# Optimization experiments

Hardware: AMD Instinct MI355X
Metric: run time of the kernel (lower is better)

The kernel has to match this reference:

```python
import jax, jax.numpy as jnp
import numpy as np

B, C, H, W = 16, 3, 384, 1280
EPS = 1e-7


def setup_inputs() -> dict:
    key = jax.random.key(0)
    k1, k2, k3, k4 = jax.random.split(key, 4)
    source_image = jax.random.normal(k1, (B, C, H, W), jnp.float32)
    depth_map = jax.random.uniform(k2, (B, 1, H, W), jnp.float32, minval=0.1, maxval=80.0)
    pose = 0.05 * jax.random.normal(k3, (B, 6), jnp.float32)
    # realistic KITTI-style pinhole intrinsics, per-batch mild perturbation
    base = jnp.array([[0.58 * W, 0.0, 0.5 * W],
                      [0.0, 1.92 * H, 0.5 * H],
                      [0.0, 0.0, 1.0]], jnp.float32)
    noise = 1.0 + 0.01 * jax.random.normal(k4, (B, 3, 3), jnp.float32)
    intrinsic = base[None] * noise  # zero entries stay zero -> invertible
    return {"source_image": source_image, "depth_map": depth_map,
            "pose": pose, "intrinsic": intrinsic}


def rot_from_axisangle(aa):
    # aa: [B,3] -> [B,3,3] (Rodrigues)
    theta = jnp.linalg.norm(aa, axis=-1, keepdims=True)  # [B,1]
    axis = aa / (theta + EPS)
    c = jnp.cos(theta)
    s = jnp.sin(theta)
    t = 1.0 - c
    x, y, z = axis[:, 0:1], axis[:, 1:2], axis[:, 2:3]
    row0 = jnp.concatenate([t * x * x + c, t * x * y - s * z, t * z * x + s * y], axis=1)
    row1 = jnp.concatenate([t * x * y + s * z, t * y * y + c, t * y * z - s * x], axis=1)
    row2 = jnp.concatenate([t * z * x - s * y, t * y * z + s * x, t * z * z + c], axis=1)
    return jnp.stack([row0, row1, row2], axis=1)  # [B,3,3]


def bilinear_grid_sample(img, gx, gy):
    # img: [B,C,H,W]; gx,gy: [B,H,W] in [-1,1]; align_corners=True, padding zeros
    Bc, Cc, Hc, Wc = img.shape
    x = (gx + 1.0) * 0.5 * (Wc - 1)
    y = (gy + 1.0) * 0.5 * (Hc - 1)
    x0 = jnp.floor(x)
    y0 = jnp.floor(y)
    x1 = x0 + 1.0
    y1 = y0 + 1.0
    wx1 = x - x0
    wx0 = 1.0 - wx1
    wy1 = y - y0
    wy0 = 1.0 - wy1
    imgf = img.reshape(Bc, Cc, Hc * Wc)

    def gather(xi, yi):
        inb = ((xi >= 0) & (xi <= Wc - 1) & (yi >= 0) & (yi <= Hc - 1)).astype(img.dtype)
        xc = jnp.clip(xi, 0, Wc - 1).astype(jnp.int32)
        yc = jnp.clip(yi, 0, Hc - 1).astype(jnp.int32)
        idx = (yc * Wc + xc).reshape(Bc, 1, -1)
        vals = jnp.take_along_axis(imgf, jnp.broadcast_to(idx, (Bc, Cc, idx.shape[-1])), axis=2)
        return vals.reshape(Bc, Cc, Hc, Wc) * inb[:, None]

    out = (gather(x0, y0) * (wx0 * wy0)[:, None]
           + gather(x1, y0) * (wx1 * wy0)[:, None]
           + gather(x0, y1) * (wx0 * wy1)[:, None]
           + gather(x1, y1) * (wx1 * wy1)[:, None])
    return out


def reference(source_image, depth_map, pose, intrinsic):
    Bb, _, Hh, Ww = depth_map.shape
    # pixel grid, homogeneous [H,W,3] = (x, y, 1)
    ys, xs = jnp.meshgrid(jnp.arange(Hh, dtype=depth_map.dtype),
                          jnp.arange(Ww, dtype=depth_map.dtype), indexing='ij')
    pix = jnp.stack([xs, ys, jnp.ones_like(xs)], axis=-1)  # [H,W,3]
    # backproject: K^{-1} @ pix * depth
    inv_K = jnp.linalg.inv(intrinsic)  # [B,3,3]
    cam = jnp.einsum('bij,hwj->bhwi', inv_K, pix)  # [B,H,W,3]
    frustum = cam * jnp.transpose(depth_map, (0, 2, 3, 1))  # [B,H,W,3]
    # rigid transform
    R = rot_from_axisangle(pose[:, :3])  # [B,3,3]
    t = pose[:, 3:]  # [B,3]
    points = jnp.einsum('bij,bhwj->bhwi', R, frustum) + t[:, None, None, :]
    # project with K
    coord = jnp.einsum('bij,bhwj->bhwi', intrinsic, points)  # [B,H,W,3]
    z = coord[..., 2] + EPS
    px = coord[..., 0] / z
    py = coord[..., 1] / z
    gx = px / (Ww - 1) * 2.0 - 1.0
    gy = py / (Hh - 1) * 2.0 - 1.0
    return bilinear_grid_sample(source_image, gx, gy)
```

## Files before the change

kernel.cpp:

```cpp
#include <hip/hip_runtime.h>
#include <hip/hip_fp16.h>

#define B_ 16
#define C_ 3
#define H_ 384
#define W_ 1280
#define HW_ (H_*W_)
#define EPS_ 1e-7f

#define WP_ 1284
#define HP_ 386
#define NXCD_ 8

#define BANDS_ (W_/256)
#define RTILES_ (H_/2)
#define NBLK3_ (BANDS_*RTILES_*B_)
#define CPX3_  (NBLK3_/NXCD_)

#define PADPB_ (2*WP_ + 4*H_)
#define NPAD_  (B_*PADPB_)

typedef float v2f __attribute__((ext_vector_type(2)));
typedef float v4f __attribute__((ext_vector_type(4)));

__device__ __forceinline__ v2f load2(const float* p) {
  v2f r; __builtin_memcpy(&r, p, 8); return r;
}
__device__ __forceinline__ uint4 load16u(const void* p) {
  uint4 r; __builtin_memcpy(&r, p, 16); return r;
}
__device__ __forceinline__ v4f ntload4(const float* p) {
  return __builtin_nontemporal_load((const v4f*)p);
}
__device__ __forceinline__ void storent2(float* p, float a, float b) {
  v2f r; r.x = a; r.y = b;
  __builtin_nontemporal_store(r, (v2f*)p);
}
__device__ __forceinline__ unsigned pack2(float a, float b) {
  __half2 h = __floats2half2_rn(a, b);
  unsigned u; __builtin_memcpy(&u, &h, 4); return u;
}

__device__ __forceinline__ void mat3mul(const float* A, const float* Bm, float* C) {
  #pragma unroll
  for (int i = 0; i < 3; i++)
    #pragma unroll
    for (int j = 0; j < 3; j++)
      C[i*3+j] = A[i*3+0]*Bm[0*3+j] + A[i*3+1]*Bm[1*3+j] + A[i*3+2]*Bm[2*3+j];
}

__device__ void compute_MT(const float* __restrict__ pose,
                           const float* __restrict__ intr,
                           int b, float* M, float* T)
{
  float K[9];
  #pragma unroll
  for (int i = 0; i < 9; i++) K[i] = intr[b*9 + i];
  float aa0 = pose[b*6 + 0], aa1 = pose[b*6 + 1], aa2 = pose[b*6 + 2];
  float t0  = pose[b*6 + 3], t1  = pose[b*6 + 4], t2  = pose[b*6 + 5];

  float theta = sqrtf(aa0*aa0 + aa1*aa1 + aa2*aa2);
  float invn  = 1.0f / (theta + EPS_);
  float x = aa0*invn, y = aa1*invn, z = aa2*invn;
  float c = cosf(theta), s = sinf(theta), t = 1.0f - c;
  float R[9] = {
    t*x*x + c,   t*x*y - s*z, t*z*x + s*y,
    t*x*y + s*z, t*y*y + c,   t*y*z - s*x,
    t*z*x - s*y, t*y*z + s*x, t*z*z + c
  };

  float a = K[0], bb = K[1], cc = K[2];
  float d = K[3], e  = K[4], f  = K[5];
  float g = K[6], h  = K[7], ii = K[8];
  float A0 = e*ii - f*h, A1 = f*g - d*ii, A2 = d*h - e*g;
  float id = 1.0f / (a*A0 + bb*A1 + cc*A2);
  float iK[9] = {
    A0*id, (cc*h - bb*ii)*id, (bb*f - cc*e)*id,
    A1*id, (a*ii - cc*g)*id,  (cc*d - a*f)*id,
    A2*id, (bb*g - a*h)*id,   (a*e  - bb*d)*id
  };

  float KR[9];
  mat3mul(K, R, KR);
  mat3mul(KR, iK, M);
  T[0] = K[0]*t0 + K[1]*t1 + K[2]*t2;
  T[1] = K[3]*t0 + K[4]*t1 + K[5]*t2;
  T[2] = K[6]*t0 + K[7]*t1 + K[8]*t2;
}

__global__ __launch_bounds__(256) void pad_kernel(unsigned long long* __restrict__ ws)
{
  int tid = blockIdx.x * 256 + threadIdx.x;
  if (tid >= NPAD_) return;
  int b = tid / PADPB_;
  int k = tid - b * PADPB_;
  int row, col;
  if (k < WP_)            { row = 0;       col = k; }
  else if (k < 2*WP_)     { row = HP_ - 1; col = k - WP_; }
  else {
    int kk = k - 2*WP_;
    row = (kk >> 2) + 1;
    int c4 = kk & 3;
    col = (c4 < 2) ? c4 : (WP_ - 4 + c4);
  }
  ws[(size_t)(b * HP_ + row) * WP_ + col] = 0ULL;
}

__global__ __launch_bounds__(256) void repack_kernel(
    const float* __restrict__ src, uint4* __restrict__ ws)
{
  int tg = blockIdx.x * 256 + threadIdx.x;
  int b  = tg / (HW_/4);
  int rq = tg - b * (HW_/4);
  int p  = rq * 4;
  int y  = p / W_;
  int x  = p - y * W_;
  const float* s = src + (size_t)b * 3 * HW_ + p;
  v4f c0 = ntload4(s);
  v4f c1 = ntload4(s + HW_);
  v4f c2 = ntload4(s + 2*HW_);
  uint4 o0, o1;
  o0.x = pack2(c0.x, c1.x); o0.y = pack2(c2.x, 0.0f);
  o0.z = pack2(c0.y, c1.y); o0.w = pack2(c2.y, 0.0f);
  o1.x = pack2(c0.z, c1.z); o1.y = pack2(c2.z, 0.0f);
  o1.z = pack2(c0.w, c1.w); o1.w = pack2(c2.w, 0.0f);
  size_t slot = (size_t)(b * HP_ + y + 1) * WP_ + (x + 2);
  ws[slot >> 1]       = o0;
  ws[(slot >> 1) + 1] = o1;
}

__global__ __launch_bounds__(256) void warp2_kernel(
    const uint4* __restrict__ pk,
    const float* __restrict__ depth,
    const float* __restrict__ pose,
    const float* __restrict__ intr,
    float* __restrict__ out)
{
  __shared__ float sp[12];

  int l = blockIdx.x;
  int w = (l & (NXCD_-1)) * CPX3_ + (l >> 3);
  int rt   = w % RTILES_;
  int tmp  = w / RTILES_;
  int band = tmp % BANDS_;
  int b    = tmp / BANDS_;

  int t  = threadIdx.x;
  int rr = t >> 7;
  int cp = t & 127;
  int j0 = band * 256 + 2*cp;
  int i  = rt * 2 + rr;

  v2f dq = load2(depth + (size_t)b * HW_ + (size_t)i * W_ + j0);

  if (t == 0) {
    float M[9], T[3];
    compute_MT(pose, intr, b, M, T);
    #pragma unroll
    for (int k = 0; k < 9; k++) sp[k] = M[k];
    #pragma unroll
    for (int k = 0; k < 3; k++) sp[9 + k] = T[k];
  }
  __syncthreads();
  float m00 = sp[0], m01 = sp[1], m02 = sp[2];
  float m10 = sp[3], m11 = sp[4], m12 = sp[5];
  float m20 = sp[6], m21 = sp[7], m22 = sp[8];
  float T0  = sp[9], T1  = sp[10], T2 = sp[11];

  float yf = (float)i;
  float bx = m01*yf + m02;
  float by = m11*yf + m12;
  float bz = m21*yf + m22;

  const char* pkb = (const char*)pk;
  const float Wm1 = (float)(W_-1), Hm1 = (float)(H_-1);
  int rowbase = b * HP_;

  float xfA = (float)j0;
  float dA  = dq.x;
  float czA = (m20*xfA + bz)*dA + T2;
  float ivA = __builtin_amdgcn_rcpf(czA + EPS_);
  float pxA = ((m00*xfA + bx)*dA + T0) * ivA;
  float pyA = ((m10*xfA + by)*dA + T1) * ivA;
  float x0A = floorf(pxA), y0A = floorf(pyA);
  float fx1A = pxA - x0A, fx0A = 1.0f - fx1A;
  float fy1A = pyA - y0A, fy0A = 1.0f - fy1A;
  float wx0A = (x0A >= 0.0f      && x0A <= Wm1) ? fx0A : 0.0f;
  float wx1A = (x0A+1.0f >= 0.0f && x0A+1.0f <= Wm1) ? fx1A : 0.0f;
  float wy0A = (y0A >= 0.0f      && y0A <= Hm1) ? fy0A : 0.0f;
  float wy1A = (y0A+1.0f >= 0.0f && y0A+1.0f <= Hm1) ? fy1A : 0.0f;
  float w00A = wx0A*wy0A, w01A = wx1A*wy0A, w10A = wx0A*wy1A, w11A = wx1A*wy1A;
  int xbA = (int)fminf(fmaxf(x0A, -1.0f), Wm1);
  int ybA = (int)fminf(fmaxf(y0A, -1.0f), Hm1);
  size_t offA0 = ((size_t)(rowbase + ybA + 1) * WP_ + (xbA + 2)) * 8;

  float xfB = (float)(j0 + 1);
  float dB  = dq.y;
  float czB = (m20*xfB + bz)*dB + T2;
  float ivB = __builtin_amdgcn_rcpf(czB + EPS_);
  float pxB = ((m00*xfB + bx)*dB + T0) * ivB;
  float pyB = ((m10*xfB + by)*dB + T1) * ivB;
  float x0B = floorf(pxB), y0B = floorf(pyB);
  float fx1B = pxB - x0B, fx0B = 1.0f - fx1B;
  float fy1B = pyB - y0B, fy0B = 1.0f - fy1B;
  float wx0B = (x0B >= 0.0f      && x0B <= Wm1) ? fx0B : 0.0f;
  float wx1B = (x0B+1.0f >= 0.0f && x0B+1.0f <= Wm1) ? fx1B : 0.0f;
  float wy0B = (y0B >= 0.0f      && y0B <= Hm1) ? fy0B : 0.0f;
  float wy1B = (y0B+1.0f >= 0.0f && y0B+1.0f <= Hm1) ? fy1B : 0.0f;
  float w00B = wx0B*wy0B, w01B = wx1B*wy0B, w10B = wx0B*wy1B, w11B = wx1B*wy1B;
  int xbB = (int)fminf(fmaxf(x0B, -1.0f), Wm1);
  int ybB = (int)fminf(fmaxf(y0B, -1.0f), Hm1);
  size_t offB0 = ((size_t)(rowbase + ybB + 1) * WP_ + (xbB + 2)) * 8;

  uint4 RA0 = load16u(pkb + offA0);
  uint4 RA1 = load16u(pkb + offA0 + (size_t)WP_*8);
  uint4 RB0 = load16u(pkb + offB0);
  uint4 RB1 = load16u(pkb + offB0 + (size_t)WP_*8);
  __builtin_amdgcn_sched_barrier(0);

  float2 A00 = __half22float2(*(const __half2*)&RA0.x);
  float  A02 = __low2float  (*(const __half2*)&RA0.y);
  float2 A01 = __half22float2(*(const __half2*)&RA0.z);
  float  A03 = __low2float  (*(const __half2*)&RA0.w);
  float2 A10 = __half22float2(*(const __half2*)&RA1.x);
  float  A12 = __low2float  (*(const __half2*)&RA1.y);
  float2 A11 = __half22float2(*(const __half2*)&RA1.z);
  float  A13 = __low2float  (*(const __half2*)&RA1.w);
  float vA0 = A00.x*w00A + A01.x*w01A + A10.x*w10A + A11.x*w11A;
  float vA1 = A00.y*w00A + A01.y*w01A + A10.y*w10A + A11.y*w11A;
  float vA2 = A02  *w00A + A03  *w01A + A12  *w10A + A13  *w11A;

  float2 B00 = __half22float2(*(const __half2*)&RB0.x);
  float  B02 = __low2float  (*(const __half2*)&RB0.y);
  float2 B01 = __half22float2(*(const __half2*)&RB0.z);
  float  B03 = __low2float  (*(const __half2*)&RB0.w);
  float2 B10 = __half22float2(*(const __half2*)&RB1.x);
  float  B12 = __low2float  (*(const __half2*)&RB1.y);
  float2 B11 = __half22float2(*(const __half2*)&RB1.z);
  float  B13 = __low2float  (*(const __half2*)&RB1.w);
  float vB0 = B00.x*w00B + B01.x*w01B + B10.x*w10B + B11.x*w11B;
  float vB1 = B00.y*w00B + B01.y*w01B + B10.y*w10B + B11.y*w11B;
  float vB2 = B02  *w00B + B03  *w01B + B12  *w10B + B13  *w11B;

  size_t sb = (size_t)b * C_ * HW_;
  size_t op = (size_t)i * W_ + j0;
  storent2(out + sb + op,                   vA0, vB0);
  storent2(out + sb + HW_ + op,             vA1, vB1);
  storent2(out + sb + 2*(size_t)HW_ + op,   vA2, vB2);
}

__global__ __launch_bounds__(256) void warp_fb_kernel(
    const float* __restrict__ src,
    const float* __restrict__ depth,
    const float* __restrict__ pose,
    const float* __restrict__ intr,
    float* __restrict__ out)
{
  __shared__ float sp[12];
  int b = blockIdx.y;
  if (threadIdx.x == 0) {
    float M[9], T[3];
    compute_MT(pose, intr, b, M, T);
    #pragma unroll
    for (int k = 0; k < 9; k++) sp[k] = M[k];
    #pragma unroll
    for (int k = 0; k < 3; k++) sp[9 + k] = T[k];
  }
  __syncthreads();
  float m00 = sp[0], m01 = sp[1], m02 = sp[2];
  float m10 = sp[3], m11 = sp[4], m12 = sp[5];
  float m20 = sp[6], m21 = sp[7], m22 = sp[8];
  float T0  = sp[9], T1  = sp[10], T2 = sp[11];

  int p = blockIdx.x * 256 + threadIdx.x;
  int j = p % W_;
  int i = p / W_;

  float d  = depth[(size_t)b * HW_ + p];
  float xf = (float)j, yf = (float)i;
  float cx = (m00*xf + m01*yf + m02)*d + T0;
  float cy = (m10*xf + m11*yf + m12)*d + T1;
  float cz = (m20*xf + m21*yf + m22)*d + T2;
  float inv = 1.0f / (cz + EPS_);
  float px = cx * inv, py = cy * inv;

  float x0f = floorf(px), y0f = floorf(py);
  float x1f = x0f + 1.0f, y1f = y0f + 1.0f;
  float wx1 = px - x0f, wx0 = 1.0f - wx1;
  float wy1 = py - y0f, wy0 = 1.0f - wy1;
  float mx0 = (x0f >= 0.0f && x0f <= (float)(W_-1)) ? 1.0f : 0.0f;
  float mx1 = (x1f >= 0.0f && x1f <= (float)(W_-1)) ? 1.0f : 0.0f;
  float my0 = (y0f >= 0.0f && y0f <= (float)(H_-1)) ? 1.0f : 0.0f;
  float my1 = (y1f >= 0.0f && y1f <= (float)(H_-1)) ? 1.0f : 0.0f;
  int xc0 = (int)fminf(fmaxf(x0f, 0.0f), (float)(W_-1));
  int xc1 = (int)fminf(fmaxf(x1f, 0.0f), (float)(W_-1));
  int yc0 = (int)fminf(fmaxf(y0f, 0.0f), (float)(H_-1));
  int yc1 = (int)fminf(fmaxf(y1f, 0.0f), (float)(H_-1));
  float w00 = wx0*wy0*mx0*my0;
  float w01 = wx1*wy0*mx1*my0;
  float w10 = wx0*wy1*mx0*my1;
  float w11 = wx1*wy1*mx1*my1;
  int base = xc0 < (W_-2) ? xc0 : (W_-2);
  bool s0 = (xc0 == base);
  bool s1 = (xc1 == base + 1);
  float wax = (s0 ? w00 : 0.0f) + (s1 ? 0.0f : w01);
  float way = (s0 ? 0.0f : w00) + (s1 ? w01 : 0.0f);
  float wbx = (s0 ? w10 : 0.0f) + (s1 ? 0.0f : w11);
  float wby = (s0 ? 0.0f : w10) + (s1 ? w11 : 0.0f);
  int rb0 = yc0*W_ + base;
  int rb1 = yc1*W_ + base;

  size_t sb = (size_t)b * C_ * HW_;
  const float* s0p = src + sb;
  const float* s1p = s0p + HW_;
  const float* s2p = s1p + HW_;
  v2f a0 = load2(s0p + rb0);
  v2f b0 = load2(s0p + rb1);
  v2f a1 = load2(s1p + rb0);
  v2f b1 = load2(s1p + rb1);
  v2f a2 = load2(s2p + rb0);
  v2f b2 = load2(s2p + rb1);
  float v0 = a0.x*wax + a0.y*way + b0.x*wbx + b0.y*wby;
  float v1 = a1.x*wax + a1.y*way + b1.x*wbx + b1.y*wby;
  float v2 = a2.x*wax + a2.y*way + b2.x*wbx + b2.y*wby;
  size_t op = (size_t)p;
  __builtin_nontemporal_store(v0, &out[sb + op]);
  __builtin_nontemporal_store(v1, &out[sb + HW_ + op]);
  __builtin_nontemporal_store(v2, &out[sb + 2*(size_t)HW_ + op]);
}

extern "C" void kernel_launch(void* const* d_in, const int* in_sizes, int n_in,
                              void* d_out, int out_size, void* d_ws, size_t ws_size,
                              hipStream_t stream) {
  const float* src   = (const float*)d_in[0];
  const float* depth = (const float*)d_in[1];
  const float* pose  = (const float*)d_in[2];
  const float* intr  = (const float*)d_in[3];
  float* out = (float*)d_out;

  const size_t need = (size_t)B_ * HP_ * WP_ * 8;
  if (d_ws != nullptr && ws_size >= need) {
    pad_kernel<<<dim3((NPAD_ + 255)/256), 256, 0, stream>>>((unsigned long long*)d_ws);
    repack_kernel<<<dim3(B_*HW_/4/256), 256, 0, stream>>>(src, (uint4*)d_ws);
    warp2_kernel<<<dim3(NBLK3_), 256, 0, stream>>>((const uint4*)d_ws, depth, pose, intr, out);
  } else {
    dim3 grid(HW_ / 256, B_);
    warp_fb_kernel<<<grid, 256, 0, stream>>>(src, depth, pose, intr, out);
  }
}
```

Before: 231.4 us.

## Fold border padding into repack and process four pixels per thread in warp

Removes the separate padding kernel launch by having the first threads of the repack kernel also zero the workspace border. The warp kernel now handles four consecutive pixels per thread (4-row tiles of 256 columns), using 16-byte depth loads and 16-byte nontemporal output stores, and issues eight gathers per thread before consuming them. This reduces the launch count and per-pixel overhead and raises memory-level parallelism, at the cost of higher register pressure and half as many blocks.

```diff
diff --git a/kernel.cpp b/kernel.cpp
--- a/kernel.cpp
+++ b/kernel.cpp
@@ -12,10 +12,11 @@
 #define HP_ 386
 #define NXCD_ 8
 
-#define BANDS_ (W_/256)
-#define RTILES_ (H_/2)
-#define NBLK3_ (BANDS_*RTILES_*B_)
-#define CPX3_  (NBLK3_/NXCD_)
+#define COLS_ 256
+#define BANDS_ (W_/COLS_)
+#define RTILES_ (H_/4)
+#define NBLK4_ (BANDS_*RTILES_*B_)
+#define CPX4_  (NBLK4_/NXCD_)
 
 #define PADPB_ (2*WP_ + 4*H_)
 #define NPAD_  (B_*PADPB_)
@@ -31,10 +32,6 @@
 }
 __device__ __forceinline__ v4f ntload4(const float* p) {
   return __builtin_nontemporal_load((const v4f*)p);
-}
-__device__ __forceinline__ void storent2(float* p, float a, float b) {
-  v2f r; r.x = a; r.y = b;
-  __builtin_nontemporal_store(r, (v2f*)p);
 }
 __device__ __forceinline__ unsigned pack2(float a, float b) {
   __half2 h = __floats2half2_rn(a, b);
@@ -88,28 +85,26 @@
   T[2] = K[6]*t0 + K[7]*t1 + K[8]*t2;
 }
 
-__global__ __launch_bounds__(256) void pad_kernel(unsigned long long* __restrict__ ws)
-{
-  int tid = blockIdx.x * 256 + threadIdx.x;
-  if (tid >= NPAD_) return;
-  int b = tid / PADPB_;
-  int k = tid - b * PADPB_;
-  int row, col;
-  if (k < WP_)            { row = 0;       col = k; }
-  else if (k < 2*WP_)     { row = HP_ - 1; col = k - WP_; }
-  else {
-    int kk = k - 2*WP_;
-    row = (kk >> 2) + 1;
-    int c4 = kk & 3;
-    col = (c4 < 2) ? c4 : (WP_ - 4 + c4);
-  }
-  ws[(size_t)(b * HP_ + row) * WP_ + col] = 0ULL;
-}
-
 __global__ __launch_bounds__(256) void repack_kernel(
     const float* __restrict__ src, uint4* __restrict__ ws)
 {
   int tg = blockIdx.x * 256 + threadIdx.x;
+
+  if (tg < NPAD_) {
+    int pb = tg / PADPB_;
+    int k  = tg - pb * PADPB_;
+    int row, col;
+    if (k < WP_)            { row = 0;       col = k; }
+    else if (k < 2*WP_)     { row = HP_ - 1; col = k - WP_; }
+    else {
+      int kk = k - 2*WP_;
+      row = (kk >> 2) + 1;
+      int c4 = kk & 3;
+      col = (c4 < 2) ? c4 : (WP_ - 4 + c4);
+    }
+    ((unsigned long long*)ws)[(size_t)(pb * HP_ + row) * WP_ + col] = 0ULL;
+  }
+
   int b  = tg / (HW_/4);
   int rq = tg - b * (HW_/4);
   int p  = rq * 4;
@@ -139,19 +134,18 @@
   __shared__ float sp[12];
 
   int l = blockIdx.x;
-  int w = (l & (NXCD_-1)) * CPX3_ + (l >> 3);
+  int w = (l & (NXCD_-1)) * CPX4_ + (l >> 3);
   int rt   = w % RTILES_;
   int tmp  = w / RTILES_;
   int band = tmp % BANDS_;
   int b    = tmp / BANDS_;
 
   int t  = threadIdx.x;
-  int rr = t >> 7;
-  int cp = t & 127;
-  int j0 = band * 256 + 2*cp;
-  int i  = rt * 2 + rr;
-
-  v2f dq = load2(depth + (size_t)b * HW_ + (size_t)i * W_ + j0);
+  int rr = t >> 6;
+  int j0 = band * COLS_ + (t & 63) * 4;
+  int i  = rt * 4 + rr;
+
+  v4f dq = *(const v4f*)(depth + (size_t)b * HW_ + (size_t)i * W_ + j0);
 
   if (t == 0) {
     float M[9], T[3];
@@ -176,77 +170,58 @@
   const float Wm1 = (float)(W_-1), Hm1 = (float)(H_-1);
   int rowbase = b * HP_;
 
-  float xfA = (float)j0;
-  float dA  = dq.x;
-  float czA = (m20*xfA + bz)*dA + T2;
-  float ivA = __builtin_amdgcn_rcpf(czA + EPS_);
-  float pxA = ((m00*xfA + bx)*dA + T0) * ivA;
-  float pyA = ((m10*xfA + by)*dA + T1) * ivA;
-  float x0A = floorf(pxA), y0A = floorf(pyA);
-  float fx1A = pxA - x0A, fx0A = 1.0f - fx1A;
-  float fy1A = pyA - y0A, fy0A = 1.0f - fy1A;
-  float wx0A = (x0A >= 0.0f      && x0A <= Wm1) ? fx0A : 0.0f;
-  float wx1A = (x0A+1.0f >= 0.0f && x0A+1.0f <= Wm1) ? fx1A : 0.0f;
-  float wy0A = (y0A >= 0.0f      && y0A <= Hm1) ? fy0A : 0.0f;
-  float wy1A = (y0A+1.0f >= 0.0f && y0A+1.0f <= Hm1) ? fy1A : 0.0f;
-  float w00A = wx0A*wy0A, w01A = wx1A*wy0A, w10A = wx0A*wy1A, w11A = wx1A*wy1A;
-  int xbA = (int)fminf(fmaxf(x0A, -1.0f), Wm1);
-  int ybA = (int)fminf(fmaxf(y0A, -1.0f), Hm1);
-  size_t offA0 = ((size_t)(rowbase + ybA + 1) * WP_ + (xbA + 2)) * 8;
-
-  float xfB = (float)(j0 + 1);
-  float dB  = dq.y;
-  float czB = (m20*xfB + bz)*dB + T2;
-  float ivB = __builtin_amdgcn_rcpf(czB + EPS_);
-  float pxB = ((m00*xfB + bx)*dB + T0) * ivB;
-  float pyB = ((m10*xfB + by)*dB + T1) * ivB;
-  float x0B = floorf(pxB), y0B = floorf(pyB);
-  float fx1B = pxB - x0B, fx0B = 1.0f - fx1B;
-  float fy1B = pyB - y0B, fy0B = 1.0f - fy1B;
-  float wx0B = (x0B >= 0.0f      && x0B <= Wm1) ? fx0B : 0.0f;
-  float wx1B = (x0B+1.0f >= 0.0f && x0B+1.0f <= Wm1) ? fx1B : 0.0f;
-  float wy0B = (y0B >= 0.0f      && y0B <= Hm1) ? fy0B : 0.0f;
-  float wy1B = (y0B+1.0f >= 0.0f && y0B+1.0f <= Hm1) ? fy1B : 0.0f;
-  float w00B = wx0B*wy0B, w01B = wx1B*wy0B, w10B = wx0B*wy1B, w11B = wx1B*wy1B;
-  int xbB = (int)fminf(fmaxf(x0B, -1.0f), Wm1);
-  int ybB = (int)fminf(fmaxf(y0B, -1.0f), Hm1);
-  size_t offB0 = ((size_t)(rowbase + ybB + 1) * WP_ + (xbB + 2)) * 8;
-
-  uint4 RA0 = load16u(pkb + offA0);
-  uint4 RA1 = load16u(pkb + offA0 + (size_t)WP_*8);
-  uint4 RB0 = load16u(pkb + offB0);
-  uint4 RB1 = load16u(pkb + offB0 + (size_t)WP_*8);
+  float w00[4], w01[4], w10[4], w11[4];
+  size_t off0[4];
+  #pragma unroll
+  for (int q = 0; q < 4; q++) {
+    float xf = (float)(j0 + q);
+    float d  = dq[q];
+    float cz = (m20*xf + bz)*d + T2;
+    float iv = __builtin_amdgcn_rcpf(cz + EPS_);
+    float px = ((m00*xf + bx)*d + T0) * iv;
+    float py = ((m10*xf + by)*d + T1) * iv;
+    float x0 = floorf(px), y0 = floorf(py);
+    float fx1 = px - x0, fx0 = 1.0f - fx1;
+    float fy1 = py - y0, fy0 = 1.0f - fy1;
+    float wx0 = (x0 >= 0.0f      && x0 <= Wm1) ? fx0 : 0.0f;
+    float wx1 = (x0+1.0f >= 0.0f && x0+1.0f <= Wm1) ? fx1 : 0.0f;
+    float wy0 = (y0 >= 0.0f      && y0 <= Hm1) ? fy0 : 0.0f;
+    float wy1 = (y0+1.0f >= 0.0f && y0+1.0f <= Hm1) ? fy1 : 0.0f;
+    w00[q] = wx0*wy0; w01[q] = wx1*wy0; w10[q] = wx0*wy1; w11[q] = wx1*wy1;
+    int xb = (int)fminf(fmaxf(x0, -1.0f), Wm1);
+    int yb = (int)fminf(fmaxf(y0, -1.0f), Hm1);
+    off0[q] = ((size_t)(rowbase + yb + 1) * WP_ + (xb + 2)) * 8;
+  }
+
+  uint4 R0[4], R1[4];
+  #pragma unroll
+  for (int q = 0; q < 4; q++) {
+    R0[q] = load16u(pkb + off0[q]);
+    R1[q] = load16u(pkb + off0[q] + (size_t)WP_*8);
+  }
   __builtin_amdgcn_sched_barrier(0);
 
-  float2 A00 = __half22float2(*(const __half2*)&RA0.x);
-  float  A02 = __low2float  (*(const __half2*)&RA0.y);
-  float2 A01 = __half22float2(*(const __half2*)&RA0.z);
-  float  A03 = __low2float  (*(const __half2*)&RA0.w);
-  float2 A10 = __half22float2(*(const __half2*)&RA1.x);
-  float  A12 = __low2float  (*(const __half2*)&RA1.y);
-  float2 A11 = __half22float2(*(const __half2*)&RA1.z);
-  float  A13 = __low2float  (*(const __half2*)&RA1.w);
-  float vA0 = A00.x*w00A + A01.x*w01A + A10.x*w10A + A11.x*w11A;
-  float vA1 = A00.y*w00A + A01.y*w01A + A10.y*w10A + A11.y*w11A;
-  float vA2 = A02  *w00A + A03  *w01A + A12  *w10A + A13  *w11A;
-
-  float2 B00 = __half22float2(*(const __half2*)&RB0.x);
-  float  B02 = __low2float  (*(const __half2*)&RB0.y);
-  float2 B01 = __half22float2(*(const __half2*)&RB0.z);
-  float  B03 = __low2float  (*(const __half2*)&RB0.w);
-  float2 B10 = __half22float2(*(const __half2*)&RB1.x);
-  float  B12 = __low2float  (*(const __half2*)&RB1.y);
-  float2 B11 = __half22float2(*(const __half2*)&RB1.z);
-  float  B13 = __low2float  (*(const __half2*)&RB1.w);
-  float vB0 = B00.x*w00B + B01.x*w01B + B10.x*w10B + B11.x*w11B;
-  float vB1 = B00.y*w00B + B01.y*w01B + B10.y*w10B + B11.y*w11B;
-  float vB2 = B02  *w00B + B03  *w01B + B12  *w10B + B13  *w11B;
+  v4f o0, o1, o2;
+  #pragma unroll
+  for (int q = 0; q < 4; q++) {
+    float2 A00 = __half22float2(*(const __half2*)&R0[q].x);
+    float  A02 = __low2float  (*(const __half2*)&R0[q].y);
+    float2 A01 = __half22float2(*(const __half2*)&R0[q].z);
+    float  A03 = __low2float  (*(const __half2*)&R0[q].w);
+    float2 A10 = __half22float2(*(const __half2*)&R1[q].x);
+    float  A12 = __low2float  (*(const __half2*)&R1[q].y);
+    float2 A11 = __half22float2(*(const __half2*)&R1[q].z);
+    float  A13 = __low2float  (*(const __half2*)&R1[q].w);
+    o0[q] = A00.x*w00[q] + A01.x*w01[q] + A10.x*w10[q] + A11.x*w11[q];
+    o1[q] = A00.y*w00[q] + A01.y*w01[q] + A10.y*w10[q] + A11.y*w11[q];
+    o2[q] = A02  *w00[q] + A03  *w01[q] + A12  *w10[q] + A13  *w11[q];
+  }
 
   size_t sb = (size_t)b * C_ * HW_;
   size_t op = (size_t)i * W_ + j0;
-  storent2(out + sb + op,                   vA0, vB0);
-  storent2(out + sb + HW_ + op,             vA1, vB1);
-  storent2(out + sb + 2*(size_t)HW_ + op,   vA2, vB2);
+  __builtin_nontemporal_store(o0, (v4f*)(out + sb + op));
+  __builtin_nontemporal_store(o1, (v4f*)(out + sb + HW_ + op));
+  __builtin_nontemporal_store(o2, (v4f*)(out + sb + 2*(size_t)HW_ + op));
 }
 
 __global__ __launch_bounds__(256) void warp_fb_kernel(
@@ -340,9 +315,8 @@
 
   const size_t need = (size_t)B_ * HP_ * WP_ * 8;
   if (d_ws != nullptr && ws_size >= need) {
-    pad_kernel<<<dim3((NPAD_ + 255)/256), 256, 0, stream>>>((unsigned long long*)d_ws);
     repack_kernel<<<dim3(B_*HW_/4/256), 256, 0, stream>>>(src, (uint4*)d_ws);
-    warp2_kernel<<<dim3(NBLK3_), 256, 0, stream>>>((const uint4*)d_ws, depth, pose, intr, out);
+    warp2_kernel<<<dim3(NBLK4_), 256, 0, stream>>>((const uint4*)d_ws, depth, pose, intr, out);
   } else {
     dim3 grid(HW_ / 256, B_);
     warp_fb_kernel<<<grid, 256, 0, stream>>>(src, depth, pose, intr, out);
```

Result: no change. 233.2 us (+0.8%).
